# Performance work log

Measured on AMD Instinct MI355X. Metric: run time of the kernel, lower is better.

Reference implementation:

```python
import jax, jax.numpy as jnp
import numpy as np


def _sage_conv(h_src, h_dst, src, dst, W_neigh, W_self, b, n_dst):
    # mean aggregation over in-neighbors of each dst node
    msg = h_src[src]                                             # [E, F]
    s = jax.ops.segment_sum(msg, dst, num_segments=n_dst)        # [n_dst, F]
    deg = jax.ops.segment_sum(jnp.ones_like(dst, dtype=h_src.dtype), dst,
                              num_segments=n_dst)                # [n_dst]
    h_neigh = s / jnp.maximum(deg, 1.0)[:, None]
    # DGL SAGEConv (mean): fc_self(h_dst) + fc_neigh(h_neigh) + bias
    return h_dst @ W_self + h_neigh @ W_neigh + b


def setup_inputs() -> dict:
    key = jax.random.key(0)
    ks = jax.random.split(key, 10)
    N1, N2, N3 = 200000, 40000, 8000
    E1, E2 = 1280000, 256000
    IN, H, C = 128, 256, 47
    return {
        "x": jax.random.normal(ks[0], (N1, IN), dtype=jnp.float32),
        "src1": jax.random.randint(ks[1], (E1,), 0, N1, dtype=jnp.int32),
        "dst1": jax.random.randint(ks[2], (E1,), 0, N2, dtype=jnp.int32),
        "src2": jax.random.randint(ks[3], (E2,), 0, N2, dtype=jnp.int32),
        "dst2": jax.random.randint(ks[4], (E2,), 0, N3, dtype=jnp.int32),
        "n_dst1": N2,
        "n_dst2": N3,
        "W_self1": jax.random.normal(ks[5], (IN, H), dtype=jnp.float32) * (1.0 / np.sqrt(IN)),
        "W_neigh1": jax.random.normal(ks[6], (IN, H), dtype=jnp.float32) * (1.0 / np.sqrt(IN)),
        "b1": jnp.zeros((H,), dtype=jnp.float32),
        "W_self2": jax.random.normal(ks[7], (H, C), dtype=jnp.float32) * (1.0 / np.sqrt(H)),
        "W_neigh2": jax.random.normal(ks[8], (H, C), dtype=jnp.float32) * (1.0 / np.sqrt(H)),
        "b2": jnp.zeros((C,), dtype=jnp.float32),
    }


def reference(x, src1, dst1, src2, dst2, n_dst1, n_dst2,
              W_self1, W_neigh1, b1, W_self2, W_neigh2, b2):
    h_dst = x[:n_dst1]                                            # [N2, IN]
    h = _sage_conv(x, h_dst, src1, dst1, W_neigh1, W_self1, b1, n_dst1)
    h = jax.nn.relu(h)                                            # [N2, H]
    h_dst2 = h[:n_dst2]                                           # [N3, H]
    out = _sage_conv(h, h_dst2, src2, dst2, W_neigh2, W_self2, b2, n_dst2)
    return out                                                    # [N3, C]
```

## Files before the change

### kernel.cpp

```cpp
#include <hip/hip_runtime.h>
#include <hip/hip_bf16.h>
#include <cstddef>


#define N1_SRC 200000
#define N2_DST 40000
#define N2_PAD 40064
#define N3_DST 8000
#define IN_F 128
#define H_F 256
#define C_F 47

#define BSHIFT 7
#define SRCB 18
#define NB1 313
#define NB2 63
#define CAP 6144

#define K1_CAST_BLOCKS 3500
#define K3_CAST_BLOCKS 1500
#define K4_CAST_BLOCKS 1250
#define K3_BASE_F4 3584000
#define K4_BASE_F4 5120000

typedef short bf16x8 __attribute__((ext_vector_type(8)));
typedef float f32x4 __attribute__((ext_vector_type(4)));

__device__ __forceinline__ float bf2f(ushort u) {
    union { uint i; float f; } v; v.i = ((uint)u) << 16; return v.f;
}
__device__ __forceinline__ ushort f2bf(float f) {
    union { float f; uint i; } v; v.f = f;
    uint r = v.i + 0x7FFF + ((v.i >> 16) & 1);
    return (ushort)(r >> 16);
}
__device__ __forceinline__ uint pack2(float lo, float hi) {
    return (uint)f2bf(lo) | ((uint)f2bf(hi) << 16);
}
__device__ __forceinline__ void acc8(float* a, uint4 v) {
    a[0] += bf2f((ushort)(v.x & 0xffff)); a[1] += bf2f((ushort)(v.x >> 16));
    a[2] += bf2f((ushort)(v.y & 0xffff)); a[3] += bf2f((ushort)(v.y >> 16));
    a[4] += bf2f((ushort)(v.z & 0xffff)); a[5] += bf2f((ushort)(v.z >> 16));
    a[6] += bf2f((ushort)(v.w & 0xffff)); a[7] += bf2f((ushort)(v.w >> 16));
}
__device__ __forceinline__ void cast4(const float4* __restrict__ in4,
                                      ushort4* __restrict__ out4, int idx) {
    float4 v = in4[idx];
    ushort4 o;
    o.x = f2bf(v.x); o.y = f2bf(v.y); o.z = f2bf(v.z); o.w = f2bf(v.w);
    out4[idx] = o;
}


#define K1_CSR (1 + H_F + 64 + 1)

__global__ __launch_bounds__(256) void k1_prep_cast(
    const float* __restrict__ x, ushort* __restrict__ xb,
    int* __restrict__ gcur1, int* __restrict__ gcur2,
    const float* __restrict__ Wself1, const float* __restrict__ Wneigh1,
    ushort* __restrict__ WT1,
    const float* __restrict__ Wself2, const float* __restrict__ Wneigh2,
    ushort* __restrict__ WT2,
    const float* __restrict__ b2, float* __restrict__ bias2p) {
    int bx = blockIdx.x, t = threadIdx.x;
    if (bx >= K1_CSR) {
        int base = (bx - K1_CSR) * 1024 + t;
#pragma unroll
        for (int j = 0; j < 4; ++j)
            cast4((const float4*)x, (ushort4*)xb, base + j * 256);
        return;
    }
    if (bx == 0) {
        for (int i = t; i < NB1; i += 256) gcur1[i] = i * CAP;
        for (int i = t; i < NB2; i += 256) gcur2[i] = i * CAP;
        return;
    }
    bx -= 1;
    if (bx < H_F) {
        int n = bx;
        for (int k = t; k < 2 * IN_F; k += 256) {
            float v = (k < IN_F) ? Wself1[(size_t)k * H_F + n]
                                 : Wneigh1[(size_t)(k - IN_F) * H_F + n];
            WT1[(size_t)n * (2 * IN_F) + k] = f2bf(v);
        }
        return;
    }
    bx -= H_F;
    if (bx < 64) {
        int n = bx;
        for (int k = t; k < 2 * H_F; k += 256) {
            float v = 0.f;
            if (n < C_F) v = (k < H_F) ? Wself2[(size_t)k * C_F + n]
                                       : Wneigh2[(size_t)(k - H_F) * C_F + n];
            WT2[(size_t)n * (2 * H_F) + k] = f2bf(v);
        }
        return;
    }
    bx -= 64;
    if (bx == 0 && t < 64) bias2p[t] = (t < C_F) ? b2[t] : 0.f;
}


#define K3_CSR (NB1 + NB2)

__global__ __launch_bounds__(256) void k3_pass1_cast(
    const float* __restrict__ x, ushort* __restrict__ xb,
    const int* __restrict__ src1, const int* __restrict__ dst1,
    int* __restrict__ gcur1, uint* __restrict__ temp1, int E1,
    const int* __restrict__ src2, const int* __restrict__ dst2,
    int* __restrict__ gcur2, uint* __restrict__ temp2, int E2) {
    __shared__ int cnt[NB1];
    __shared__ int rnk[NB1];
    __shared__ int gbase[NB1];
    int bx = blockIdx.x, t = threadIdx.x;
    if (bx >= K3_CSR) {
        int base = K3_BASE_F4 + (bx - K3_CSR) * 1024 + t;
#pragma unroll
        for (int j = 0; j < 4; ++j)
            cast4((const float4*)x, (ushort4*)xb, base + j * 256);
        return;
    }
    int L = (bx >= NB1);
    int pb = L ? bx - NB1 : bx;
    const int* src = L ? src2 : src1;
    const int* dst = L ? dst2 : dst1;
    int* gcur = L ? gcur2 : gcur1;
    uint* temp = L ? temp2 : temp1;
    int E = L ? E2 : E1;
    int e0 = pb * 4096;
    if (e0 >= E) return;
    for (int i = t; i < NB1; i += 256) { cnt[i] = 0; rnk[i] = 0; }
    __syncthreads();
#pragma unroll
    for (int i = 0; i < 16; ++i) {
        int e = e0 + i * 256 + t;
        if (e < E) atomicAdd(&cnt[dst[e] >> BSHIFT], 1);
    }
    __syncthreads();
    for (int b = t; b < NB1; b += 256) {
        int c = cnt[b];
        gbase[b] = c ? atomicAdd(&gcur[b], c) : 0;
    }
    __syncthreads();
#pragma unroll
    for (int i = 0; i < 16; ++i) {
        int e = e0 + i * 256 + t;
        if (e < E) {
            int d = dst[e];
            int b = d >> BSHIFT;
            int r = atomicAdd(&rnk[b], 1);
            uint val = ((uint)(d & 127) << SRCB) | (uint)src[e];
            temp[gbase[b] + r] = val;
        }
    }
}


#define K4_CSR (NB1 + NB2)

__global__ __launch_bounds__(256) void k4_pass2_cast(
    const float* __restrict__ x, ushort* __restrict__ xb,
    const uint* __restrict__ temp1, const int* __restrict__ gcur1,
    int* __restrict__ off1, int* __restrict__ deg1, int* __restrict__ edges1,
    const uint* __restrict__ temp2, const int* __restrict__ gcur2,
    int* __restrict__ off2, int* __restrict__ deg2, int* __restrict__ edges2) {
    constexpr int DPB = 128;
    __shared__ int cnt[DPB];
    __shared__ int scn[DPB];
    __shared__ int obase[DPB];
    __shared__ int rnk[DPB];
    int bx = blockIdx.x, t = threadIdx.x;
    if (bx >= K4_CSR) {
        int base = K4_BASE_F4 + (bx - K4_CSR) * 1024 + t;
#pragma unroll
        for (int j = 0; j < 4; ++j)
            cast4((const float4*)x, (ushort4*)xb, base + j * 256);
        return;
    }
    int L = (bx >= NB1);
    int lb = L ? bx - NB1 : bx;
    const uint* temp = L ? temp2 : temp1;
    const int* gcur = L ? gcur2 : gcur1;
    int* offsets = L ? off2 : off1;
    int* degs = L ? deg2 : deg1;
    int* edges = L ? edges2 : edges1;
    int nd = L ? N3_DST : N2_DST;
    int dbase = lb << BSHIFT;
    int beg = lb * CAP;
    int end = gcur[lb];
    if (t < DPB) { cnt[t] = 0; rnk[t] = 0; }
    __syncthreads();
    for (int i = beg + t; i < end; i += 256) {
        atomicAdd(&cnt[temp[i] >> SRCB], 1);
    }
    __syncthreads();
    int v = (t < DPB) ? cnt[t] : 0;
    if (t < DPB) scn[t] = v;
    __syncthreads();
    for (int off = 1; off < DPB; off <<= 1) {
        int tv = (t >= off && t < DPB) ? scn[t - off] : 0;
        __syncthreads();
        if (t < DPB) scn[t] += tv;
        __syncthreads();
    }
    if (t < DPB) {
        int ob = beg + scn[t] - v;
        obase[t] = ob;
        if (dbase + t < nd) { offsets[dbase + t] = ob; degs[dbase + t] = v; }
    }
    __syncthreads();
    for (int i = beg + t; i < end; i += 256) {
        uint val = temp[i];
        int dlow = (int)(val >> SRCB);
        int s = (int)(val & ((1u << SRCB) - 1));
        int r = atomicAdd(&rnk[dlow], 1);
        edges[obase[dlow] + r] = s;
    }
}


__global__ __launch_bounds__(256) void gather_mean_f128(
    const ushort* __restrict__ xb, const int* __restrict__ edges,
    const int* __restrict__ offsets, const int* __restrict__ degs,
    ushort* __restrict__ outb) {
    int d = (blockIdx.x << 2) | (threadIdx.x >> 6);
    int lane = threadIdx.x & 63;
    int eslot = lane >> 4, lpos = lane & 15;
    int beg = offsets[d];
    int deg = degs[d];
    int end = beg + deg;
    float a[8] = {};
    int i = beg;
    for (; i + 16 <= end; i += 16) {
        int e0 = edges[i + eslot];
        int e1 = edges[i + 4 + eslot];
        int e2 = edges[i + 8 + eslot];
        int e3 = edges[i + 12 + eslot];
        uint4 v0 = ((const uint4*)(xb + (size_t)e0 * IN_F))[lpos];
        uint4 v1 = ((const uint4*)(xb + (size_t)e1 * IN_F))[lpos];
        uint4 v2 = ((const uint4*)(xb + (size_t)e2 * IN_F))[lpos];
        uint4 v3 = ((const uint4*)(xb + (size_t)e3 * IN_F))[lpos];
        acc8(a, v0); acc8(a, v1); acc8(a, v2); acc8(a, v3);
    }
    for (; i < end; i += 4) {
        if (i + eslot < end) {
            int e = edges[i + eslot];
            uint4 v = ((const uint4*)(xb + (size_t)e * IN_F))[lpos];
            acc8(a, v);
        }
    }
#pragma unroll
    for (int j = 0; j < 8; ++j) {
        a[j] += __shfl_xor(a[j], 16);
        a[j] += __shfl_xor(a[j], 32);
    }
    if (eslot == 0) {
        float inv = 1.0f / fmaxf((float)deg, 1.0f);
        uint4 o;
        o.x = pack2(a[0] * inv, a[1] * inv);
        o.y = pack2(a[2] * inv, a[3] * inv);
        o.z = pack2(a[4] * inv, a[5] * inv);
        o.w = pack2(a[6] * inv, a[7] * inv);
        ((uint4*)(outb + (size_t)d * IN_F))[lpos] = o;
    }
}

__global__ __launch_bounds__(256) void gather_mean_f256(
    const ushort* __restrict__ hb, const int* __restrict__ edges,
    const int* __restrict__ offsets, const int* __restrict__ degs,
    ushort* __restrict__ outb) {
    int d = (blockIdx.x << 2) | (threadIdx.x >> 6);
    int lane = threadIdx.x & 63;
    int eslot = lane >> 5, lpos = lane & 31;
    int beg = offsets[d];
    int deg = degs[d];
    int end = beg + deg;
    float a[8] = {};
    int i = beg;
    for (; i + 8 <= end; i += 8) {
        int e0 = edges[i + eslot];
        int e1 = edges[i + 2 + eslot];
        int e2 = edges[i + 4 + eslot];
        int e3 = edges[i + 6 + eslot];
        uint4 v0 = ((const uint4*)(hb + (size_t)e0 * H_F))[lpos];
        uint4 v1 = ((const uint4*)(hb + (size_t)e1 * H_F))[lpos];
        uint4 v2 = ((const uint4*)(hb + (size_t)e2 * H_F))[lpos];
        uint4 v3 = ((const uint4*)(hb + (size_t)e3 * H_F))[lpos];
        acc8(a, v0); acc8(a, v1); acc8(a, v2); acc8(a, v3);
    }
    for (; i < end; i += 2) {
        if (i + eslot < end) {
            int e = edges[i + eslot];
            uint4 v = ((const uint4*)(hb + (size_t)e * H_F))[lpos];
            acc8(a, v);
        }
    }
#pragma unroll
    for (int j = 0; j < 8; ++j) {
        a[j] += __shfl_xor(a[j], 32);
    }
    if (eslot == 0) {
        float inv = 1.0f / fmaxf((float)deg, 1.0f);
        uint4 o;
        o.x = pack2(a[0] * inv, a[1] * inv);
        o.y = pack2(a[2] * inv, a[3] * inv);
        o.z = pack2(a[4] * inv, a[5] * inv);
        o.w = pack2(a[6] * inv, a[7] * inv);
        ((uint4*)(outb + (size_t)d * H_F))[lpos] = o;
    }
}


__global__ __launch_bounds__(256) void sage_mfma_gemm128(
    const ushort* __restrict__ Aself, const ushort* __restrict__ Aneigh,
    const ushort* __restrict__ WT, const float* __restrict__ bias,
    ushort* __restrict__ Cout) {
    constexpr int LDL = 72;
    __shared__ __align__(16) ushort A_lds[128 * LDL];
    __shared__ __align__(16) ushort B_lds[128 * LDL];
    int t = threadIdx.x;
    int bn = blockIdx.x * 128, bm = blockIdx.y * 128;
    int lane = t & 63, w = t >> 6;
    int wr = w >> 1, wc = w & 1;
    int ln = lane & 15, kh = lane >> 4;
    f32x4 acc[4][4] = {};
    for (int kt0 = 0; kt0 < 256; kt0 += 64) {
#pragma unroll
        for (int c = 0; c < 4; ++c) {
            int id = c * 256 + t;
            int row = id >> 3;
            int kc = (id & 7) * 8;
            int k = kt0 + kc;
            const ushort* sa = (k < IN_F)
                                   ? Aself + (size_t)(bm + row) * IN_F + k
                                   : Aneigh + (size_t)(bm + row) * IN_F + (k - IN_F);
            *(float4*)&A_lds[row * LDL + kc] = *(const float4*)sa;
            *(float4*)&B_lds[row * LDL + kc] =
                *(const float4*)(WT + (size_t)(bn + row) * 256 + k);
        }
        __syncthreads();
#pragma unroll
        for (int kt = 0; kt < 2; ++kt) {
            bf16x8 aF[4], bF[4];
#pragma unroll
            for (int m = 0; m < 4; ++m)
                aF[m] = *(const bf16x8*)&A_lds[(wr * 64 + m * 16 + ln) * LDL + kt * 32 + kh * 8];
#pragma unroll
            for (int n = 0; n < 4; ++n)
                bF[n] = *(const bf16x8*)&B_lds[(wc * 64 + n * 16 + ln) * LDL + kt * 32 + kh * 8];
#pragma unroll
            for (int m = 0; m < 4; ++m)
#pragma unroll
                for (int n = 0; n < 4; ++n)
                    acc[m][n] = __builtin_amdgcn_mfma_f32_16x16x32_bf16(
                        aF[m], bF[n], acc[m][n], 0, 0, 0);
        }
        __syncthreads();
    }
#pragma unroll
    for (int m = 0; m < 4; ++m) {
#pragma unroll
        for (int n = 0; n < 4; ++n) {
            int col = bn + wc * 64 + n * 16 + ln;
            float bv = bias[col];
#pragma unroll
            for (int r = 0; r < 4; ++r) {
                int row = bm + wr * 64 + m * 16 + kh * 4 + r;
                float v = fmaxf(acc[m][n][r] + bv, 0.f);
                Cout[(size_t)row * H_F + col] = f2bf(v);
            }
        }
    }
}


template <int K, int KSELF, bool RELU, bool OUTF32>
__global__ __launch_bounds__(256) void sage_mfma_gemm(
    const ushort* __restrict__ Aself, const ushort* __restrict__ Aneigh,
    const ushort* __restrict__ WT, const float* __restrict__ bias,
    void* __restrict__ Cout, int ldc, int ncols) {
    constexpr int KN = K - KSELF;
    constexpr int LDL = K + 8;
    __shared__ __align__(16) ushort A_lds[64 * LDL];
    __shared__ __align__(16) ushort B_lds[64 * LDL];
    int t = threadIdx.x;
    int bn = blockIdx.x * 64, bm = blockIdx.y * 64;
    constexpr int CPR = K / 8;
    constexpr int ITER = 64 * CPR / 256;
#pragma unroll
    for (int c = 0; c < ITER; ++c) {
        int id = c * 256 + t;
        int row = id / CPR;
        int kc = (id % CPR) * 8;
        const ushort* sa = (kc < KSELF)
                               ? Aself + (size_t)(bm + row) * KSELF + kc
                               : Aneigh + (size_t)(bm + row) * KN + (kc - KSELF);
        float4 av = *(const float4*)sa;
        float4 bv = *(const float4*)(WT + (size_t)(bn + row) * K + kc);
        *(float4*)&A_lds[row * LDL + kc] = av;
        *(float4*)&B_lds[row * LDL + kc] = bv;
    }
    __syncthreads();
    int lane = t & 63, w = t >> 6;
    int wr = w >> 1, wc = w & 1;
    int ln = lane & 15, kh = lane >> 4;
    const ushort* Ab = &A_lds[(wr * 32 + ln) * LDL + kh * 8];
    const ushort* Bb = &B_lds[(wc * 32 + ln) * LDL + kh * 8];
    f32x4 acc00 = {0.f, 0.f, 0.f, 0.f};
    f32x4 acc01 = {0.f, 0.f, 0.f, 0.f};
    f32x4 acc10 = {0.f, 0.f, 0.f, 0.f};
    f32x4 acc11 = {0.f, 0.f, 0.f, 0.f};
#pragma unroll
    for (int kt = 0; kt < K / 32; ++kt) {
        bf16x8 a0 = *(const bf16x8*)(Ab + kt * 32);
        bf16x8 a1 = *(const bf16x8*)(Ab + 16 * LDL + kt * 32);
        bf16x8 b0 = *(const bf16x8*)(Bb + kt * 32);
        bf16x8 b1 = *(const bf16x8*)(Bb + 16 * LDL + kt * 32);
        acc00 = __builtin_amdgcn_mfma_f32_16x16x32_bf16(a0, b0, acc00, 0, 0, 0);
        acc01 = __builtin_amdgcn_mfma_f32_16x16x32_bf16(a0, b1, acc01, 0, 0, 0);
        acc10 = __builtin_amdgcn_mfma_f32_16x16x32_bf16(a1, b0, acc10, 0, 0, 0);
        acc11 = __builtin_amdgcn_mfma_f32_16x16x32_bf16(a1, b1, acc11, 0, 0, 0);
    }
    f32x4 accs[2][2] = {{acc00, acc01}, {acc10, acc11}};
#pragma unroll
    for (int m = 0; m < 2; ++m) {
#pragma unroll
        for (int n = 0; n < 2; ++n) {
            int col = bn + wc * 32 + n * 16 + ln;
            float bv = bias[col];
#pragma unroll
            for (int r = 0; r < 4; ++r) {
                int row = bm + wr * 32 + m * 16 + kh * 4 + r;
                float v = accs[m][n][r] + bv;
                if (RELU) v = fmaxf(v, 0.f);
                if (OUTF32) {
                    if (col < ncols) ((float*)Cout)[(size_t)row * ncols + col] = v;
                } else {
                    ((ushort*)Cout)[(size_t)row * ldc + col] = f2bf(v);
                }
            }
        }
    }
}


static inline char* carve(char*& p, size_t bytes) {
    char* r = p;
    p += (bytes + 255) & ~(size_t)255;
    return r;
}

extern "C" void kernel_launch(void* const* d_in, const int* in_sizes, int n_in,
                              void* d_out, int out_size, void* d_ws, size_t ws_size,
                              hipStream_t stream) {
    const float* x        = (const float*)d_in[0];
    const int*   src1     = (const int*)d_in[1];
    const int*   dst1     = (const int*)d_in[2];
    const int*   src2     = (const int*)d_in[3];
    const int*   dst2     = (const int*)d_in[4];
    const float* W_self1  = (const float*)d_in[7];
    const float* W_neigh1 = (const float*)d_in[8];
    const float* b1       = (const float*)d_in[9];
    const float* W_self2  = (const float*)d_in[10];
    const float* W_neigh2 = (const float*)d_in[11];
    const float* b2       = (const float*)d_in[12];
    float* out = (float*)d_out;

    const int E1 = in_sizes[1];
    const int E2 = in_sizes[3];

    char* p = (char*)d_ws;
    ushort* xb       = (ushort*)carve(p, (size_t)N1_SRC * IN_F * 2);
    ushort* hb       = (ushort*)carve(p, (size_t)N2_PAD * H_F * 2);
    ushort* hneighb  = (ushort*)carve(p, (size_t)N2_PAD * IN_F * 2);
    ushort* hneigh2b = (ushort*)carve(p, (size_t)N3_DST * H_F * 2);
    int*    edges2   = (int*)carve(p, (size_t)NB2 * CAP * 4);
    int*    off1     = (int*)carve(p, (size_t)N2_DST * 4);
    int*    off2     = (int*)carve(p, (size_t)N3_DST * 4);
    int*    deg1     = (int*)carve(p, (size_t)N2_DST * 4);
    int*    deg2     = (int*)carve(p, (size_t)N3_DST * 4);
    int*    gcur1    = (int*)carve(p, (size_t)NB1 * 4);
    int*    gcur2    = (int*)carve(p, (size_t)NB2 * 4);
    ushort* WT1      = (ushort*)carve(p, (size_t)H_F * (2 * IN_F) * 2);
    ushort* WT2      = (ushort*)carve(p, (size_t)64 * (2 * H_F) * 2);
    float*  bias2p   = (float*)carve(p, 64 * 4);
    uint* temp1 = (uint*)hneighb;
    uint* temp2 = temp1 + (size_t)NB1 * CAP;
    int* edges1 = (int*)hb;

    k1_prep_cast<<<K1_CSR + K1_CAST_BLOCKS, 256, 0, stream>>>(
        x, xb, gcur1, gcur2,
        W_self1, W_neigh1, WT1, W_self2, W_neigh2, WT2, b2, bias2p);

    k3_pass1_cast<<<K3_CSR + K3_CAST_BLOCKS, 256, 0, stream>>>(
        x, xb, src1, dst1, gcur1, temp1, E1, src2, dst2, gcur2, temp2, E2);

    k4_pass2_cast<<<K4_CSR + K4_CAST_BLOCKS, 256, 0, stream>>>(
        x, xb, temp1, gcur1, off1, deg1, edges1,
        temp2, gcur2, off2, deg2, edges2);

    gather_mean_f128<<<N2_DST / 4, 256, 0, stream>>>(xb, edges1, off1, deg1, hneighb);
    {
        dim3 grid(H_F / 128, N2_PAD / 128);
        sage_mfma_gemm128<<<grid, 256, 0, stream>>>(xb, hneighb, WT1, b1, hb);
    }

    gather_mean_f256<<<N3_DST / 4, 256, 0, stream>>>(hb, edges2, off2, deg2, hneigh2b);
    {
        dim3 grid(1, N3_DST / 64);
        sage_mfma_gemm<512, 256, false, true><<<grid, 256, 0, stream>>>(
            hb, hneigh2b, WT2, bias2p, out, C_F, C_F);
    }
}
```

Baseline: 148.1 us.

## Reorder layer-2 SAGE: project before aggregating to shrink gathered feature width

Layer 2 now multiplies every layer-1 output row by W_neigh2 first, producing a 64-wide bf16 projection, and then mean-aggregates those projected rows. It no longer gathers 256-wide hidden rows and multiplies afterwards. A single dual-role GEMM kernel computes the neighbor projection for all 40k nodes and the self term plus bias for the 8000 output rows. A new gather kernel then adds the scaled neighbor mean into the output. This cuts gather traffic per edge by a factor of four, but the projection GEMM now runs over five times as many rows, and the projected values are rounded to bf16 before averaging.

```diff
diff --git a/kernel.cpp b/kernel.cpp
--- a/kernel.cpp
+++ b/kernel.cpp
@@ -60,7 +60,7 @@
     const float* __restrict__ Wself1, const float* __restrict__ Wneigh1,
     ushort* __restrict__ WT1,
     const float* __restrict__ Wself2, const float* __restrict__ Wneigh2,
-    ushort* __restrict__ WT2,
+    ushort* __restrict__ WT2n, ushort* __restrict__ WT2s,
     const float* __restrict__ b2, float* __restrict__ bias2p) {
     int bx = blockIdx.x, t = threadIdx.x;
     if (bx >= K1_CSR) {
@@ -88,11 +88,14 @@
     bx -= H_F;
     if (bx < 64) {
         int n = bx;
-        for (int k = t; k < 2 * H_F; k += 256) {
-            float v = 0.f;
-            if (n < C_F) v = (k < H_F) ? Wself2[(size_t)k * C_F + n]
-                                       : Wneigh2[(size_t)(k - H_F) * C_F + n];
-            WT2[(size_t)n * (2 * H_F) + k] = f2bf(v);
+        for (int k = t; k < H_F; k += 256) {
+            float vn = 0.f, vs = 0.f;
+            if (n < C_F) {
+                vn = Wneigh2[(size_t)k * C_F + n];
+                vs = Wself2[(size_t)k * C_F + n];
+            }
+            WT2n[(size_t)n * H_F + k] = f2bf(vn);
+            WT2s[(size_t)n * H_F + k] = f2bf(vs);
         }
         return;
     }
@@ -265,51 +268,6 @@
     }
 }
 
-__global__ __launch_bounds__(256) void gather_mean_f256(
-    const ushort* __restrict__ hb, const int* __restrict__ edges,
-    const int* __restrict__ offsets, const int* __restrict__ degs,
-    ushort* __restrict__ outb) {
-    int d = (blockIdx.x << 2) | (threadIdx.x >> 6);
-    int lane = threadIdx.x & 63;
-    int eslot = lane >> 5, lpos = lane & 31;
-    int beg = offsets[d];
-    int deg = degs[d];
-    int end = beg + deg;
-    float a[8] = {};
-    int i = beg;
-    for (; i + 8 <= end; i += 8) {
-        int e0 = edges[i + eslot];
-        int e1 = edges[i + 2 + eslot];
-        int e2 = edges[i + 4 + eslot];
-        int e3 = edges[i + 6 + eslot];
-        uint4 v0 = ((const uint4*)(hb + (size_t)e0 * H_F))[lpos];
-        uint4 v1 = ((const uint4*)(hb + (size_t)e1 * H_F))[lpos];
-        uint4 v2 = ((const uint4*)(hb + (size_t)e2 * H_F))[lpos];
-        uint4 v3 = ((const uint4*)(hb + (size_t)e3 * H_F))[lpos];
-        acc8(a, v0); acc8(a, v1); acc8(a, v2); acc8(a, v3);
-    }
-    for (; i < end; i += 2) {
-        if (i + eslot < end) {
-            int e = edges[i + eslot];
-            uint4 v = ((const uint4*)(hb + (size_t)e * H_F))[lpos];
-            acc8(a, v);
-        }
-    }
-#pragma unroll
-    for (int j = 0; j < 8; ++j) {
-        a[j] += __shfl_xor(a[j], 32);
-    }
-    if (eslot == 0) {
-        float inv = 1.0f / fmaxf((float)deg, 1.0f);
-        uint4 o;
-        o.x = pack2(a[0] * inv, a[1] * inv);
-        o.y = pack2(a[2] * inv, a[3] * inv);
-        o.z = pack2(a[4] * inv, a[5] * inv);
-        o.w = pack2(a[6] * inv, a[7] * inv);
-        ((uint4*)(outb + (size_t)d * H_F))[lpos] = o;
-    }
-}
-
 
 __global__ __launch_bounds__(256) void sage_mfma_gemm128(
     const ushort* __restrict__ Aself, const ushort* __restrict__ Aneigh,
@@ -374,31 +332,33 @@
 }
 
 
-template <int K, int KSELF, bool RELU, bool OUTF32>
-__global__ __launch_bounds__(256) void sage_mfma_gemm(
-    const ushort* __restrict__ Aself, const ushort* __restrict__ Aneigh,
-    const ushort* __restrict__ WT, const float* __restrict__ bias,
-    void* __restrict__ Cout, int ldc, int ncols) {
-    constexpr int KN = K - KSELF;
+#define G2_NEIGH_BLKS (N2_PAD / 64)
+#define G2_SELF_BLKS (N3_DST / 64)
+
+__global__ __launch_bounds__(256) void gemm2_dual(
+    const ushort* __restrict__ hb,
+    const ushort* __restrict__ WT2n, const ushort* __restrict__ WT2s,
+    const float* __restrict__ bias2p,
+    ushort* __restrict__ y2n, float* __restrict__ out) {
+    constexpr int K = H_F;
     constexpr int LDL = K + 8;
     __shared__ __align__(16) ushort A_lds[64 * LDL];
     __shared__ __align__(16) ushort B_lds[64 * LDL];
     int t = threadIdx.x;
-    int bn = blockIdx.x * 64, bm = blockIdx.y * 64;
+    int by = blockIdx.x;
+    bool selfHalf = (by >= G2_NEIGH_BLKS);
+    int bm = selfHalf ? (by - G2_NEIGH_BLKS) * 64 : by * 64;
+    const ushort* WT = selfHalf ? WT2s : WT2n;
     constexpr int CPR = K / 8;
-    constexpr int ITER = 64 * CPR / 256;
-#pragma unroll
-    for (int c = 0; c < ITER; ++c) {
+#pragma unroll
+    for (int c = 0; c < 8; ++c) {
         int id = c * 256 + t;
         int row = id / CPR;
         int kc = (id % CPR) * 8;
-        const ushort* sa = (kc < KSELF)
-                               ? Aself + (size_t)(bm + row) * KSELF + kc
-                               : Aneigh + (size_t)(bm + row) * KN + (kc - KSELF);
-        float4 av = *(const float4*)sa;
-        float4 bv = *(const float4*)(WT + (size_t)(bn + row) * K + kc);
-        *(float4*)&A_lds[row * LDL + kc] = av;
-        *(float4*)&B_lds[row * LDL + kc] = bv;
+        *(float4*)&A_lds[row * LDL + kc] =
+            *(const float4*)(hb + (size_t)(bm + row) * K + kc);
+        *(float4*)&B_lds[row * LDL + kc] =
+            *(const float4*)(WT + (size_t)row * K + kc);
     }
     __syncthreads();
     int lane = t & 63, w = t >> 6;
@@ -426,19 +386,61 @@
     for (int m = 0; m < 2; ++m) {
 #pragma unroll
         for (int n = 0; n < 2; ++n) {
-            int col = bn + wc * 32 + n * 16 + ln;
-            float bv = bias[col];
+            int col = wc * 32 + n * 16 + ln;
 #pragma unroll
             for (int r = 0; r < 4; ++r) {
                 int row = bm + wr * 32 + m * 16 + kh * 4 + r;
-                float v = accs[m][n][r] + bv;
-                if (RELU) v = fmaxf(v, 0.f);
-                if (OUTF32) {
-                    if (col < ncols) ((float*)Cout)[(size_t)row * ncols + col] = v;
+                float v = accs[m][n][r];
+                if (selfHalf) {
+                    if (col < C_F)
+                        out[(size_t)row * C_F + col] = v + bias2p[col];
                 } else {
-                    ((ushort*)Cout)[(size_t)row * ldc + col] = f2bf(v);
+                    y2n[(size_t)row * 64 + col] = f2bf(v);
                 }
             }
+        }
+    }
+}
+
+
+__global__ __launch_bounds__(256) void gather_add_mean(
+    const ushort* __restrict__ y2n, const int* __restrict__ edges,
+    const int* __restrict__ offsets, const int* __restrict__ degs,
+    float* __restrict__ out) {
+    int d = (blockIdx.x << 2) | (threadIdx.x >> 6);
+    int lane = threadIdx.x & 63;
+    int eslot = lane >> 3, lpos = lane & 7;
+    int beg = offsets[d];
+    int deg = degs[d];
+    int end = beg + deg;
+    float a[8] = {};
+    int i = beg;
+    for (; i + 16 <= end; i += 16) {
+        int e0 = edges[i + eslot];
+        int e1 = edges[i + 8 + eslot];
+        uint4 v0 = ((const uint4*)(y2n + (size_t)e0 * 64))[lpos];
+        uint4 v1 = ((const uint4*)(y2n + (size_t)e1 * 64))[lpos];
+        acc8(a, v0); acc8(a, v1);
+    }
+    for (; i < end; i += 8) {
+        if (i + eslot < end) {
+            int e = edges[i + eslot];
+            uint4 v = ((const uint4*)(y2n + (size_t)e * 64))[lpos];
+            acc8(a, v);
+        }
+    }
+#pragma unroll
+    for (int j = 0; j < 8; ++j) {
+        a[j] += __shfl_xor(a[j], 8);
+        a[j] += __shfl_xor(a[j], 16);
+        a[j] += __shfl_xor(a[j], 32);
+    }
+    if (eslot == 0) {
+        float inv = 1.0f / fmaxf((float)deg, 1.0f);
+#pragma unroll
+        for (int j = 0; j < 8; ++j) {
+            int c = lpos * 8 + j;
+            if (c < C_F) out[(size_t)d * C_F + c] += a[j] * inv;
         }
     }
 }
@@ -473,7 +475,7 @@
     ushort* xb       = (ushort*)carve(p, (size_t)N1_SRC * IN_F * 2);
     ushort* hb       = (ushort*)carve(p, (size_t)N2_PAD * H_F * 2);
     ushort* hneighb  = (ushort*)carve(p, (size_t)N2_PAD * IN_F * 2);
-    ushort* hneigh2b = (ushort*)carve(p, (size_t)N3_DST * H_F * 2);
+    ushort* y2n      = (ushort*)carve(p, (size_t)N2_PAD * 64 * 2);
     int*    edges2   = (int*)carve(p, (size_t)NB2 * CAP * 4);
     int*    off1     = (int*)carve(p, (size_t)N2_DST * 4);
     int*    off2     = (int*)carve(p, (size_t)N3_DST * 4);
@@ -482,7 +484,8 @@
     int*    gcur1    = (int*)carve(p, (size_t)NB1 * 4);
     int*    gcur2    = (int*)carve(p, (size_t)NB2 * 4);
     ushort* WT1      = (ushort*)carve(p, (size_t)H_F * (2 * IN_F) * 2);
-    ushort* WT2      = (ushort*)carve(p, (size_t)64 * (2 * H_F) * 2);
+    ushort* WT2n     = (ushort*)carve(p, (size_t)64 * H_F * 2);
+    ushort* WT2s     = (ushort*)carve(p, (size_t)64 * H_F * 2);
     float*  bias2p   = (float*)carve(p, 64 * 4);
     uint* temp1 = (uint*)hneighb;
     uint* temp2 = temp1 + (size_t)NB1 * CAP;
@@ -490,7 +493,7 @@
 
     k1_prep_cast<<<K1_CSR + K1_CAST_BLOCKS, 256, 0, stream>>>(
         x, xb, gcur1, gcur2,
-        W_self1, W_neigh1, WT1, W_self2, W_neigh2, WT2, b2, bias2p);
+        W_self1, W_neigh1, WT1, W_self2, W_neigh2, WT2n, WT2s, b2, bias2p);
 
     k3_pass1_cast<<<K3_CSR + K3_CAST_BLOCKS, 256, 0, stream>>>(
         x, xb, src1, dst1, gcur1, temp1, E1, src2, dst2, gcur2, temp2, E2);
@@ -500,15 +503,14 @@
         temp2, gcur2, off2, deg2, edges2);
 
     gather_mean_f128<<<N2_DST / 4, 256, 0, stream>>>(xb, edges1, off1, deg1, hneighb);
+
     {
         dim3 grid(H_F / 128, N2_PAD / 128);
         sage_mfma_gemm128<<<grid, 256, 0, stream>>>(xb, hneighb, WT1, b1, hb);
     }
 
-    gather_mean_f256<<<N3_DST / 4, 256, 0, stream>>>(hb, edges2, off2, deg2, hneigh2b);
-    {
-        dim3 grid(1, N3_DST / 64);
-        sage_mfma_gemm<512, 256, false, true><<<grid, 256, 0, stream>>>(
-            hb, hneigh2b, WT2, bias2p, out, C_F, C_F);
-    }
-}
+    gemm2_dual<<<G2_NEIGH_BLKS + G2_SELF_BLKS, 256, 0, stream>>>(
+        hb, WT2n, WT2s, bias2p, y2n, out);
+
+    gather_add_mean<<<N3_DST / 4, 256, 0, stream>>>(y2n, edges2, off2, deg2, out);
+}
```

Measured after the change: 142.4 us. 1.04x faster.
